# Kernel optimization log

Measured on AMD Instinct MI355X. Metric: run time of the kernel, lower is better.

The kernel has to match this reference:

```python
import jax, jax.numpy as jnp
import numpy as np

B, K, D, H = 4, 2048, 768, 12
HD = D // H
NEG = -1e30  # stands in for -inf in the additive mask


def setup_inputs() -> dict:
    key = jax.random.key(0)
    ks = jax.random.split(key, 11)
    s = 1.0 / np.sqrt(D)
    inp = {
        "x": jax.random.normal(ks[0], (B, K, D), jnp.float32),
        "is_context": jax.random.randint(ks[1], (B, K), 0, 2) > 0,
        "Wq": jax.random.normal(ks[2], (D, D), jnp.float32) * s,
        "bq": jax.random.normal(ks[3], (D,), jnp.float32) * 0.01,
        "Wk": jax.random.normal(ks[4], (D, D), jnp.float32) * s,
        "bk": jax.random.normal(ks[5], (D,), jnp.float32) * 0.01,
        "Wv": jax.random.normal(ks[6], (D, D), jnp.float32) * s,
        "bv": jax.random.normal(ks[7], (D,), jnp.float32) * 0.01,
        "Wo": jax.random.normal(ks[8], (D, D), jnp.float32) * s,
        "bo": jax.random.normal(ks[9], (D,), jnp.float32) * 0.01,
    }
    return inp


def reference(x, is_context, Wq, bq, Wk, bk, Wv, bv, Wo, bo):
    b, k_len, d = x.shape
    scale = 1.0 / jnp.sqrt(jnp.asarray(HD, x.dtype))
    # torch nn.Linear: y = x @ W.T + b
    q = (x @ Wq.T + bq).reshape(b, k_len, H, HD).transpose(0, 2, 1, 3)  # [B,H,K,hd]
    kk = (x @ Wk.T + bk).reshape(b, k_len, H, HD).transpose(0, 2, 1, 3)
    v = (x @ Wv.T + bv).reshape(b, k_len, H, HD).transpose(0, 2, 1, 3)

    ctx = is_context  # [B,K] bool
    # allowed[b,i,j]: context rows attend only to context cols; target rows attend to all
    allowed = (ctx[:, :, None] & ctx[:, None, :]) | (~ctx)[:, :, None]  # [B,K,K]

    scores = jnp.einsum("bhqd,bhkd->bhqk", q, kk) * scale  # [B,H,K,K]
    scores = jnp.where(allowed[:, None, :, :], scores, NEG)
    attn = jax.nn.softmax(scores, axis=-1)
    out = jnp.einsum("bhqk,bhkd->bhqd", attn, v)  # [B,H,K,hd]
    out = out.transpose(0, 2, 1, 3).reshape(b, k_len, d)
    return out @ Wo.T + bo
```

## Files before the change

### kernel.cpp

```cpp
#include <hip/hip_runtime.h>
#include <hip/hip_bf16.h>

constexpr int BATCH = 4;
constexpr int SEQ   = 2048;
constexpr int DIM   = 768;
constexpr int NH    = 12;
constexpr int HDIM  = 64;

typedef __attribute__((ext_vector_type(8))) short bf16x8;
typedef __attribute__((ext_vector_type(4))) float f32x4;
typedef __attribute__((ext_vector_type(4))) short s16x4;

__device__ inline short f2bf(float f) {
    union { float f; unsigned u; } v; v.f = f;
    unsigned r = (v.u + 0x7fff + ((v.u >> 16) & 1)) >> 16;
    return (short)r;
}

__device__ inline unsigned pack_bf16x2(float a, float b) {
    union { __hip_bfloat162 h; unsigned u; } c;
    c.h = __float22bfloat162_rn(make_float2(a, b));
    return c.u;
}

__device__ inline float fast_exp2(float x) {
#if __has_builtin(__builtin_amdgcn_exp2f)
    return __builtin_amdgcn_exp2f(x);
#else
    return __expf(x * 0.6931471805599453f);
#endif
}

__device__ inline void gld16(const short* g, short* l) {
    __builtin_amdgcn_global_load_lds(
        (const __attribute__((address_space(1))) void*)g,
        (__attribute__((address_space(3))) void*)l, 16, 0, 0);
}

__device__ inline bool ctx_at(const void* p, bool isU8, int idx) {
    return isU8 ? (((const unsigned char*)p)[idx] != 0)
                : (((const int*)p)[idx] != 0);
}

__global__ __launch_bounds__(256) void prep_kernel(
    const float* __restrict__ x,  const float* __restrict__ Wq,
    const float* __restrict__ Wk, const float* __restrict__ Wv,
    const float* __restrict__ Wo,
    short* __restrict__ xb,  short* __restrict__ Wqb,
    short* __restrict__ Wkb, short* __restrict__ Wvb,
    short* __restrict__ Wob,
    const unsigned char* __restrict__ ctxm, int ctxbytes, int* __restrict__ flag) {
    const int blk = blockIdx.x;
    constexpr int XBLK = (BATCH * SEQ * DIM / 4) / 256;
    constexpr int WBLK = (DIM * DIM / 4) / 256;

    if (blk == XBLK + 4 * WBLK) {
        __shared__ int cnt;
        if (threadIdx.x == 0) cnt = 0;
        __syncthreads();
        int local = 0;
        for (int i = threadIdx.x; i < ctxbytes; i += 256)
            if ((i & 3) != 0 && ctxm[i] != 0) local++;
        atomicAdd(&cnt, local);
        __syncthreads();
        if (threadIdx.x == 0) *flag = (cnt > 0) ? 1 : 0;
        return;
    }

    const float* src; short* dst; int i;
    if (blk < XBLK) {
        src = x; dst = xb;
        i = blk * 256 + threadIdx.x;
    } else {
        const int r = blk - XBLK;
        const int w = r / WBLK;
        src = (w == 0) ? Wq : (w == 1) ? Wk : (w == 2) ? Wv : Wo;
        dst = (w == 0) ? Wqb : (w == 1) ? Wkb : (w == 2) ? Wvb : Wob;
        i = (r - w * WBLK) * 256 + threadIdx.x;
    }
    float4 v = ((const float4*)src)[i];
    s16x4 o;
    o.x = f2bf(v.x); o.y = f2bf(v.y); o.z = f2bf(v.z); o.w = f2bf(v.w);
    ((s16x4*)dst)[i] = o;
}

template <bool BF16OUT>
__global__ __launch_bounds__(256) void gemm_mfma(
    const short* __restrict__ A,
    const short* __restrict__ W0, const float* __restrict__ bias0, void* __restrict__ C0,
    const short* __restrict__ W1, const float* __restrict__ bias1, void* __restrict__ C1,
    const short* __restrict__ W2, const float* __restrict__ bias2, void* __restrict__ C2,
    float scale0) {
    constexpr int N  = DIM;
    constexpr int Kd = DIM;
    constexpr int NT = Kd / 32;

    const short* W; const float* bias; void* C; float scale;
    if (blockIdx.z == 0)      { W = W0; bias = bias0; C = C0; scale = scale0; }
    else if (blockIdx.z == 1) { W = W1; bias = bias1; C = C1; scale = 1.f; }
    else                      { W = W2; bias = bias2; C = C2; scale = 1.f; }

    const int tid  = threadIdx.x;
    const int wave = tid >> 6;
    const int lane = tid & 63;
    const int quad = lane >> 4;
    const int l16  = lane & 15;
    const int wm   = wave & 1;
    const int wn   = wave >> 1;
    const int m0   = blockIdx.y * 128;
    const int n0   = blockIdx.x * 128;

    __shared__ short As[2][128 * 32];
    __shared__ short Bs[2][128 * 32];

    const int srow = tid >> 2;
    const int gj   = (tid & 3) ^ (srow & 3);
    const short* Ag = A + (size_t)(m0 + srow) * Kd + gj * 8;
    const short* Wg = W + (size_t)(n0 + srow) * Kd + gj * 8;

    f32x4 acc[4][4] = {};

    gld16(Ag,               &As[0][tid * 8]);
    gld16(Ag + 64 * Kd,     &As[0][(tid + 256) * 8]);
    gld16(Wg,               &Bs[0][tid * 8]);
    gld16(Wg + 64 * Kd,     &Bs[0][(tid + 256) * 8]);

    const int rchunk = quad ^ (l16 & 3);

    for (int it = 0; it < NT; ++it) {
        const int cur = it & 1;
        __syncthreads();

        if (it + 1 < NT) {
            const int kt = (it + 1) * 32;
            const int nb = cur ^ 1;
            gld16(Ag + kt,           &As[nb][tid * 8]);
            gld16(Ag + kt + 64 * Kd, &As[nb][(tid + 256) * 8]);
            gld16(Wg + kt,           &Bs[nb][tid * 8]);
            gld16(Wg + kt + 64 * Kd, &Bs[nb][(tid + 256) * 8]);
        }

        bf16x8 af[4], bfr[4];
#pragma unroll
        for (int mt = 0; mt < 4; ++mt)
            af[mt] = *(const bf16x8*)&As[cur][(wm * 64 + mt * 16 + l16) * 32 + rchunk * 8];
#pragma unroll
        for (int nt = 0; nt < 4; ++nt)
            bfr[nt] = *(const bf16x8*)&Bs[cur][(wn * 64 + nt * 16 + l16) * 32 + rchunk * 8];
#pragma unroll
        for (int mt = 0; mt < 4; ++mt)
#pragma unroll
            for (int nt = 0; nt < 4; ++nt)
                acc[mt][nt] = __builtin_amdgcn_mfma_f32_16x16x32_bf16(
                    af[mt], bfr[nt], acc[mt][nt], 0, 0, 0);
    }

    float bv[4];
#pragma unroll
    for (int nt = 0; nt < 4; ++nt) bv[nt] = bias[n0 + wn * 64 + nt * 16 + l16];

#pragma unroll
    for (int mt = 0; mt < 4; ++mt)
#pragma unroll
        for (int nt = 0; nt < 4; ++nt)
#pragma unroll
            for (int reg = 0; reg < 4; ++reg) {
                const int m = m0 + wm * 64 + mt * 16 + quad * 4 + reg;
                const int n = n0 + wn * 64 + nt * 16 + l16;
                const float v = (acc[mt][nt][reg] + bv[nt]) * scale;
                if (BF16OUT) ((short*)C)[(size_t)m * N + n] = f2bf(v);
                else         ((float*)C)[(size_t)m * N + n] = v;
            }
}

__global__ __launch_bounds__(256) void vtrans_kernel(
    const short* __restrict__ Vb, short* __restrict__ Vtg) {
    const int b  = blockIdx.z;
    const int h  = blockIdx.y;
    const int k0 = blockIdx.x * 64;
    const int kl = threadIdx.x & 15;
    const int d0 = (threadIdx.x >> 4) * 4;

    s16x4 vr[4];
#pragma unroll
    for (int g = 0; g < 4; ++g)
        vr[g] = *(const s16x4*)(Vb + (size_t)(b * SEQ + k0 + g * 16 + kl) * DIM
                                + h * HDIM + d0);
#pragma unroll
    for (int i = 0; i < 4; ++i) {
        s16x4 w = {vr[0][i], vr[1][i], vr[2][i], vr[3][i]};
        *(s16x4*)(Vtg + (size_t)((b * NH + h) * HDIM + d0 + i) * SEQ + k0 + 4 * kl) = w;
    }
}

__global__ __launch_bounds__(256, 3) void attn_mfma6(
    const short* __restrict__ Qb, const short* __restrict__ Kb,
    const short* __restrict__ Vtg, const void* __restrict__ ctxp,
    const int* __restrict__ flagp, short* __restrict__ Ob) {
    const int b    = blockIdx.z;
    const int h    = blockIdx.y;
    const int q0   = blockIdx.x * 128;
    const int tid  = threadIdx.x;
    const int wave = tid >> 6;
    const int lane = tid & 63;
    const int quad = lane >> 4;
    const int l16  = lane & 15;
    const bool isU8 = (*flagp != 0);

    __shared__ short Ks[2][64 * 64];
    __shared__ short Vs[2][64 * 64];
    __shared__ short Ps[4][32 * 64];

    short* Pw = Ps[wave];

    const short* Kg = Kb + (size_t)b * SEQ * DIM + h * HDIM;
    const short* Vg = Vtg + (size_t)(b * NH + h) * HDIM * SEQ;

    const int r0 = tid >> 3;
    const int j0 = (tid & 7) ^ (r0 & 7);
    const int sw = l16 & 7;

    bf16x8 qf[2][2];
#pragma unroll
    for (int rg = 0; rg < 2; ++rg) {
        const short* qp = Qb + (size_t)(b * SEQ + q0 + wave * 32 + rg * 16 + l16) * DIM
                        + h * HDIM + quad * 8;
        qf[rg][0] = *(const bf16x8*)qp;
        qf[rg][1] = *(const bf16x8*)(qp + 32);
    }

    unsigned nmb[2][4];
#pragma unroll
    for (int rg = 0; rg < 2; ++rg)
#pragma unroll
        for (int reg = 0; reg < 4; ++reg)
            nmb[rg][reg] = ctx_at(ctxp, isU8,
                b * SEQ + q0 + wave * 32 + rg * 16 + quad * 4 + reg) ? 0u : 0xFFFFFFFFu;

    bf16x8 ones;
#pragma unroll
    for (int i = 0; i < 8; ++i) ones[i] = (short)0x3F80;

    f32x4 accl[2] = {};
    f32x4 acc[2][4] = {};

    {
        gld16(Kg + (size_t)r0 * DIM + j0 * 8,        &Ks[0][tid * 8]);
        gld16(Kg + (size_t)(r0 + 32) * DIM + j0 * 8, &Ks[0][(tid + 256) * 8]);
        gld16(Vg + (size_t)r0 * SEQ + j0 * 8,        &Vs[0][tid * 8]);
        gld16(Vg + (size_t)(r0 + 32) * SEQ + j0 * 8, &Vs[0][(tid + 256) * 8]);
    }

    constexpr int NT = SEQ / 64;
    for (int t = 0; t < NT; ++t) {
        const int k0  = t * 64;
        const int cur = t & 1;

        __syncthreads();

        if (t + 1 < NT) {
            const int kn  = k0 + 64;
            const int nxt = cur ^ 1;
            gld16(Kg + (size_t)(kn + r0) * DIM + j0 * 8,        &Ks[nxt][tid * 8]);
            gld16(Kg + (size_t)(kn + r0 + 32) * DIM + j0 * 8,   &Ks[nxt][(tid + 256) * 8]);
            gld16(Vg + (size_t)r0 * SEQ + kn + j0 * 8,          &Vs[nxt][tid * 8]);
            gld16(Vg + (size_t)(r0 + 32) * SEQ + kn + j0 * 8,   &Vs[nxt][(tid + 256) * 8]);
        }

        const short* BK = Ks[cur];
        const short* BV = Vs[cur];

        const unsigned long long kmask =
            __ballot(ctx_at(ctxp, isU8, b * SEQ + k0 + lane));
        unsigned km2[2];
#pragma unroll
        for (int gp = 0; gp < 2; ++gp) {
            const unsigned lo = (unsigned)((kmask >> (gp * 32 + l16)) & 1ull);
            const unsigned hi = (unsigned)((kmask >> (gp * 32 + 16 + l16)) & 1ull);
            km2[gp] = (lo ? 0x0000FFFFu : 0u) | (hi ? 0xFFFF0000u : 0u);
        }

        f32x4 s4[2][4] = {};
#pragma unroll
        for (int ks = 0; ks < 2; ++ks) {
            bf16x8 kf[4];
#pragma unroll
            for (int g = 0; g < 4; ++g)
                kf[g] = *(const bf16x8*)
                    &BK[(g * 16 + l16) * 64 + (((ks * 4 + quad) ^ sw)) * 8];
#pragma unroll
            for (int g = 0; g < 4; ++g) {
                s4[0][g] = __builtin_amdgcn_mfma_f32_16x16x32_bf16(qf[0][ks], kf[g], s4[0][g], 0, 0, 0);
                s4[1][g] = __builtin_amdgcn_mfma_f32_16x16x32_bf16(qf[1][ks], kf[g], s4[1][g], 0, 0, 0);
            }
        }

#pragma unroll
        for (int rg = 0; rg < 2; ++rg)
#pragma unroll
            for (int reg = 0; reg < 4; ++reg) {
                const float p0 = fast_exp2(s4[rg][0][reg]);
                const float p1 = fast_exp2(s4[rg][1][reg]);
                const float p2 = fast_exp2(s4[rg][2][reg]);
                const float p3 = fast_exp2(s4[rg][3][reg]);
                uint2 w;
                w.x = pack_bf16x2(p0, p1) & (nmb[rg][reg] | km2[0]);
                w.y = pack_bf16x2(p2, p3) & (nmb[rg][reg] | km2[1]);
                const int row = rg * 16 + quad * 4 + reg;
                const int pos = (l16 >> 1) ^ (row & 7);
                *(uint2*)&Pw[row * 64 + pos * 8 + (l16 & 1) * 4] = w;
            }

#pragma unroll
        for (int ks = 0; ks < 2; ++ks) {
            const int rpos = (ks * 4 + quad) ^ sw;
            bf16x8 pf0 = *(const bf16x8*)&Pw[l16 * 64 + rpos * 8];
            bf16x8 pf1 = *(const bf16x8*)&Pw[(16 + l16) * 64 + rpos * 8];
            accl[0] = __builtin_amdgcn_mfma_f32_16x16x32_bf16(pf0, ones, accl[0], 0, 0, 0);
            accl[1] = __builtin_amdgcn_mfma_f32_16x16x32_bf16(pf1, ones, accl[1], 0, 0, 0);
#pragma unroll
            for (int dt = 0; dt < 4; ++dt) {
                bf16x8 vf = *(const bf16x8*)
                    &BV[(dt * 16 + l16) * 64 + (((ks * 4 + quad) ^ sw)) * 8];
                acc[0][dt] = __builtin_amdgcn_mfma_f32_16x16x32_bf16(pf0, vf, acc[0][dt], 0, 0, 0);
                acc[1][dt] = __builtin_amdgcn_mfma_f32_16x16x32_bf16(pf1, vf, acc[1][dt], 0, 0, 0);
            }
        }
    }

    float inv[2][4];
#pragma unroll
    for (int rg = 0; rg < 2; ++rg)
#pragma unroll
        for (int reg = 0; reg < 4; ++reg)
            inv[rg][reg] = 1.f / accl[rg][reg];

#pragma unroll
    for (int rg = 0; rg < 2; ++rg)
#pragma unroll
        for (int dt = 0; dt < 4; ++dt)
#pragma unroll
            for (int reg = 0; reg < 4; ++reg) {
                const int q = q0 + wave * 32 + rg * 16 + quad * 4 + reg;
                Ob[(size_t)(b * SEQ + q) * DIM + h * HDIM + dt * 16 + l16] =
                    f2bf(acc[rg][dt][reg] * inv[rg][reg]);
            }
}

extern "C" void kernel_launch(void* const* d_in, const int* in_sizes, int n_in,
                              void* d_out, int out_size, void* d_ws, size_t ws_size,
                              hipStream_t stream) {
    const float* x   = (const float*)d_in[0];
    const void*  ctx = d_in[1];
    const float* Wq  = (const float*)d_in[2];
    const float* bq  = (const float*)d_in[3];
    const float* Wk  = (const float*)d_in[4];
    const float* bk  = (const float*)d_in[5];
    const float* Wv  = (const float*)d_in[6];
    const float* bv  = (const float*)d_in[7];
    const float* Wo  = (const float*)d_in[8];
    const float* bo  = (const float*)d_in[9];
    float* out = (float*)d_out;

    char* ws = (char*)d_ws;
    int* flag = (int*)ws;
    const size_t bufbf = (size_t)BATCH * SEQ * DIM * sizeof(short);
    const size_t wbuf  = (size_t)DIM * DIM * sizeof(short);
    short* xb  = (short*)(ws + 256);
    short* Qb  = (short*)(ws + 256 + bufbf);
    short* Kb  = (short*)(ws + 256 + 2 * bufbf);
    short* Vb  = (short*)(ws + 256 + 3 * bufbf);
    short* Ab  = (short*)(ws + 256 + 4 * bufbf);
    short* Vtg = (short*)(ws + 256 + 5 * bufbf);
    short* Wqb = (short*)(ws + 256 + 6 * bufbf);
    short* Wkb = (short*)(ws + 256 + 6 * bufbf + wbuf);
    short* Wvb = (short*)(ws + 256 + 6 * bufbf + 2 * wbuf);
    short* Wob = (short*)(ws + 256 + 6 * bufbf + 3 * wbuf);

    constexpr int XBLK = (BATCH * SEQ * DIM / 4) / 256;
    constexpr int WBLK = (DIM * DIM / 4) / 256;
    prep_kernel<<<XBLK + 4 * WBLK + 1, 256, 0, stream>>>(
        x, Wq, Wk, Wv, Wo, xb, Wqb, Wkb, Wvb, Wob,
        (const unsigned char*)ctx, BATCH * SEQ, flag);

    dim3 gQKV(DIM / 128, (BATCH * SEQ) / 128, 3);
    gemm_mfma<true><<<gQKV, 256, 0, stream>>>(
        xb, Wqb, bq, Qb, Wkb, bk, Kb, Wvb, bv, Vb, 0.125f * 1.4426950408889634f);

    dim3 gVt(SEQ / 64, NH, BATCH);
    vtrans_kernel<<<gVt, 256, 0, stream>>>(Vb, Vtg);

    dim3 gAttn(SEQ / 128, NH, BATCH);
    attn_mfma6<<<gAttn, 256, 0, stream>>>(Qb, Kb, Vtg, ctx, flag, Ab);

    dim3 gOut(DIM / 128, (BATCH * SEQ) / 128, 1);
    gemm_mfma<false><<<gOut, 256, 0, stream>>>(
        Ab, Wob, bo, out, Wob, bo, out, Wob, bo, out, 1.f);
}
```

Measured before the change: 260.8 us.

## Fuse V transpose into QKV GEMM epilogue and change LDS swizzle

The QKV GEMM now writes the V projection straight into the head-major transposed layout the attention kernel consumes, so the separate vtrans kernel and the intermediate V buffer are removed. The LDS XOR swizzle now keys on row pairs instead of single rows. The main loop is manually unrolled by two with constant buffer indices. This saves a kernel launch and a full read and write of V, at the cost of strided 8-byte global stores in the V epilogue.

```diff
diff --git a/kernel.cpp b/kernel.cpp
--- a/kernel.cpp
+++ b/kernel.cpp
@@ -90,7 +90,7 @@
     const short* __restrict__ W0, const float* __restrict__ bias0, void* __restrict__ C0,
     const short* __restrict__ W1, const float* __restrict__ bias1, void* __restrict__ C1,
     const short* __restrict__ W2, const float* __restrict__ bias2, void* __restrict__ C2,
-    float scale0) {
+    short* __restrict__ Vtg, float scale0) {
     constexpr int N  = DIM;
     constexpr int Kd = DIM;
     constexpr int NT = Kd / 32;
@@ -114,50 +114,77 @@
     __shared__ short Bs[2][128 * 32];
 
     const int srow = tid >> 2;
-    const int gj   = (tid & 3) ^ (srow & 3);
+    const int gj   = (tid & 3) ^ ((srow >> 1) & 3);
     const short* Ag = A + (size_t)(m0 + srow) * Kd + gj * 8;
     const short* Wg = W + (size_t)(n0 + srow) * Kd + gj * 8;
+    const int rchunk = quad ^ ((l16 >> 1) & 3);
 
     f32x4 acc[4][4] = {};
 
-    gld16(Ag,               &As[0][tid * 8]);
-    gld16(Ag + 64 * Kd,     &As[0][(tid + 256) * 8]);
-    gld16(Wg,               &Bs[0][tid * 8]);
-    gld16(Wg + 64 * Kd,     &Bs[0][(tid + 256) * 8]);
-
-    const int rchunk = quad ^ (l16 & 3);
-
-    for (int it = 0; it < NT; ++it) {
-        const int cur = it & 1;
-        __syncthreads();
-
-        if (it + 1 < NT) {
-            const int kt = (it + 1) * 32;
-            const int nb = cur ^ 1;
-            gld16(Ag + kt,           &As[nb][tid * 8]);
-            gld16(Ag + kt + 64 * Kd, &As[nb][(tid + 256) * 8]);
-            gld16(Wg + kt,           &Bs[nb][tid * 8]);
-            gld16(Wg + kt + 64 * Kd, &Bs[nb][(tid + 256) * 8]);
+    gld16(Ag,           &As[0][tid * 8]);
+    gld16(Ag + 64 * Kd, &As[0][(tid + 256) * 8]);
+    gld16(Wg,           &Bs[0][tid * 8]);
+    gld16(Wg + 64 * Kd, &Bs[0][(tid + 256) * 8]);
+
+#define GEMM_PHASE(BUF, NEXTBUF, IT)                                           \
+    {                                                                          \
+        __syncthreads();                                                       \
+        if ((IT) + 1 < NT) {                                                   \
+            const int kt = ((IT) + 1) * 32;                                    \
+            gld16(Ag + kt,           &As[NEXTBUF][tid * 8]);                   \
+            gld16(Ag + kt + 64 * Kd, &As[NEXTBUF][(tid + 256) * 8]);           \
+            gld16(Wg + kt,           &Bs[NEXTBUF][tid * 8]);                   \
+            gld16(Wg + kt + 64 * Kd, &Bs[NEXTBUF][(tid + 256) * 8]);           \
+        }                                                                      \
+        bf16x8 af[4], bfr[4];                                                  \
+        _Pragma("unroll")                                                      \
+        for (int mt = 0; mt < 4; ++mt)                                         \
+            af[mt] = *(const bf16x8*)                                          \
+                &As[BUF][(wm * 64 + mt * 16 + l16) * 32 + rchunk * 8];         \
+        _Pragma("unroll")                                                      \
+        for (int nt = 0; nt < 4; ++nt)                                         \
+            bfr[nt] = *(const bf16x8*)                                         \
+                &Bs[BUF][(wn * 64 + nt * 16 + l16) * 32 + rchunk * 8];         \
+        _Pragma("unroll")                                                      \
+        for (int mt = 0; mt < 4; ++mt)                                         \
+            _Pragma("unroll")                                                  \
+            for (int nt = 0; nt < 4; ++nt)                                     \
+                acc[mt][nt] = __builtin_amdgcn_mfma_f32_16x16x32_bf16(         \
+                    af[mt], bfr[nt], acc[mt][nt], 0, 0, 0);                    \
+    }
+
+    for (int it = 0; it < NT; it += 2) {
+        GEMM_PHASE(0, 1, it)
+        GEMM_PHASE(1, 0, it + 1)
+    }
+#undef GEMM_PHASE
+
+    float bvv[4];
+#pragma unroll
+    for (int nt = 0; nt < 4; ++nt) bvv[nt] = bias[n0 + wn * 64 + nt * 16 + l16];
+
+    if (BF16OUT && blockIdx.z == 2) {
+        const int bq     = m0 >> 11;
+        const int tile64 = (m0 & (SEQ - 1)) + wm * 64;
+        const int hh     = (n0 >> 6) + wn;
+        short* dstb = Vtg + (size_t)(bq * NH + hh) * HDIM * SEQ
+                    + tile64 + 16 * quad;
+#pragma unroll
+        for (int nt = 0; nt < 4; ++nt) {
+            const int d = nt * 16 + l16;
+            short* dst = dstb + (size_t)d * SEQ;
+#pragma unroll
+            for (int reg = 0; reg < 4; ++reg) {
+                uint2 w;
+                w.x = pack_bf16x2(acc[0][nt][reg] + bvv[nt],
+                                  acc[1][nt][reg] + bvv[nt]);
+                w.y = pack_bf16x2(acc[2][nt][reg] + bvv[nt],
+                                  acc[3][nt][reg] + bvv[nt]);
+                *(uint2*)(dst + 4 * reg) = w;
+            }
         }
-
-        bf16x8 af[4], bfr[4];
-#pragma unroll
-        for (int mt = 0; mt < 4; ++mt)
-            af[mt] = *(const bf16x8*)&As[cur][(wm * 64 + mt * 16 + l16) * 32 + rchunk * 8];
-#pragma unroll
-        for (int nt = 0; nt < 4; ++nt)
-            bfr[nt] = *(const bf16x8*)&Bs[cur][(wn * 64 + nt * 16 + l16) * 32 + rchunk * 8];
-#pragma unroll
-        for (int mt = 0; mt < 4; ++mt)
-#pragma unroll
-            for (int nt = 0; nt < 4; ++nt)
-                acc[mt][nt] = __builtin_amdgcn_mfma_f32_16x16x32_bf16(
-                    af[mt], bfr[nt], acc[mt][nt], 0, 0, 0);
-    }
-
-    float bv[4];
-#pragma unroll
-    for (int nt = 0; nt < 4; ++nt) bv[nt] = bias[n0 + wn * 64 + nt * 16 + l16];
+        return;
+    }
 
 #pragma unroll
     for (int mt = 0; mt < 4; ++mt)
@@ -167,30 +194,10 @@
             for (int reg = 0; reg < 4; ++reg) {
                 const int m = m0 + wm * 64 + mt * 16 + quad * 4 + reg;
                 const int n = n0 + wn * 64 + nt * 16 + l16;
-                const float v = (acc[mt][nt][reg] + bv[nt]) * scale;
+                const float v = (acc[mt][nt][reg] + bvv[nt]) * scale;
                 if (BF16OUT) ((short*)C)[(size_t)m * N + n] = f2bf(v);
                 else         ((float*)C)[(size_t)m * N + n] = v;
             }
-}
-
-__global__ __launch_bounds__(256) void vtrans_kernel(
-    const short* __restrict__ Vb, short* __restrict__ Vtg) {
-    const int b  = blockIdx.z;
-    const int h  = blockIdx.y;
-    const int k0 = blockIdx.x * 64;
-    const int kl = threadIdx.x & 15;
-    const int d0 = (threadIdx.x >> 4) * 4;
-
-    s16x4 vr[4];
-#pragma unroll
-    for (int g = 0; g < 4; ++g)
-        vr[g] = *(const s16x4*)(Vb + (size_t)(b * SEQ + k0 + g * 16 + kl) * DIM
-                                + h * HDIM + d0);
-#pragma unroll
-    for (int i = 0; i < 4; ++i) {
-        s16x4 w = {vr[0][i], vr[1][i], vr[2][i], vr[3][i]};
-        *(s16x4*)(Vtg + (size_t)((b * NH + h) * HDIM + d0 + i) * SEQ + k0 + 4 * kl) = w;
-    }
 }
 
 __global__ __launch_bounds__(256, 3) void attn_mfma6(
@@ -369,13 +376,12 @@
     short* xb  = (short*)(ws + 256);
     short* Qb  = (short*)(ws + 256 + bufbf);
     short* Kb  = (short*)(ws + 256 + 2 * bufbf);
-    short* Vb  = (short*)(ws + 256 + 3 * bufbf);
+    short* Vtg = (short*)(ws + 256 + 3 * bufbf);
     short* Ab  = (short*)(ws + 256 + 4 * bufbf);
-    short* Vtg = (short*)(ws + 256 + 5 * bufbf);
-    short* Wqb = (short*)(ws + 256 + 6 * bufbf);
-    short* Wkb = (short*)(ws + 256 + 6 * bufbf + wbuf);
-    short* Wvb = (short*)(ws + 256 + 6 * bufbf + 2 * wbuf);
-    short* Wob = (short*)(ws + 256 + 6 * bufbf + 3 * wbuf);
+    short* Wqb = (short*)(ws + 256 + 5 * bufbf);
+    short* Wkb = (short*)(ws + 256 + 5 * bufbf + wbuf);
+    short* Wvb = (short*)(ws + 256 + 5 * bufbf + 2 * wbuf);
+    short* Wob = (short*)(ws + 256 + 5 * bufbf + 3 * wbuf);
 
     constexpr int XBLK = (BATCH * SEQ * DIM / 4) / 256;
     constexpr int WBLK = (DIM * DIM / 4) / 256;
@@ -385,15 +391,13 @@
 
     dim3 gQKV(DIM / 128, (BATCH * SEQ) / 128, 3);
     gemm_mfma<true><<<gQKV, 256, 0, stream>>>(
-        xb, Wqb, bq, Qb, Wkb, bk, Kb, Wvb, bv, Vb, 0.125f * 1.4426950408889634f);
-
-    dim3 gVt(SEQ / 64, NH, BATCH);
-    vtrans_kernel<<<gVt, 256, 0, stream>>>(Vb, Vtg);
+        xb, Wqb, bq, Qb, Wkb, bk, Kb, Wvb, bv, nullptr, Vtg,
+        0.125f * 1.4426950408889634f);
 
     dim3 gAttn(SEQ / 128, NH, BATCH);
     attn_mfma6<<<gAttn, 256, 0, stream>>>(Qb, Kb, Vtg, ctx, flag, Ab);
 
     dim3 gOut(DIM / 128, (BATCH * SEQ) / 128, 1);
     gemm_mfma<false><<<gOut, 256, 0, stream>>>(
-        Ab, Wob, bo, out, Wob, bo, out, Wob, bo, out, 1.f);
-}
+        Ab, Wob, bo, out, Wob, bo, out, Wob, bo, out, nullptr, 1.f);
+}
```

Result: no change. 265.0 us (+1.6%).
